# Optimization experiments

Measured on AMD Instinct MI355X. Metric: run time of the kernel, lower is better.

The kernel has to match this reference:

```python
import jax, jax.numpy as jnp
import numpy as np

B, LQ, LT, D = 16, 576, 512, 768
H, DH = 12, 64
TOPK = 64
GATE_INIT = -4.0
EPS = 1e-5


def _layernorm(x, g, b):
    m = jnp.mean(x, axis=-1, keepdims=True)
    v = jnp.mean(jnp.square(x - m), axis=-1, keepdims=True)
    return (x - m) * jax.lax.rsqrt(v + EPS) * g + b


def setup_inputs() -> dict:
    key = jax.random.key(0)
    ks = jax.random.split(key, 8)
    s = D ** -0.5
    return {
        "x_q": jax.random.normal(ks[0], (B, LQ, D), jnp.float32),
        "x_kv": jax.random.normal(ks[1], (B, LT, D), jnp.float32),
        "kv_attn_mask": jnp.ones((B, LT), jnp.int32),
        "wq": jax.random.normal(ks[2], (D, D), jnp.float32) * s,
        "wk": jax.random.normal(ks[3], (D, D), jnp.float32) * s,
        "wv": jax.random.normal(ks[4], (D, D), jnp.float32) * s,
        "wo": jax.random.normal(ks[5], (D, D), jnp.float32) * s,
        "ln_q_g": jnp.ones((D,), jnp.float32),
        "ln_q_b": jnp.zeros((D,), jnp.float32),
        "ln_kv_g": jnp.ones((D,), jnp.float32),
        "ln_kv_b": jnp.zeros((D,), jnp.float32),
        "head_queries": jax.random.normal(ks[6], (H, DH), jnp.float32) * DH ** -0.5,
        "resid_logit": jnp.asarray(GATE_INIT, jnp.float32),
    }


def reference(x_q, x_kv, kv_attn_mask, wq, wk, wv, wo,
              ln_q_g, ln_q_b, ln_kv_g, ln_kv_b, head_queries, resid_logit):
    scale = DH ** -0.5
    Bc, Lq, _ = x_q.shape
    Lt = x_kv.shape[1]
    xq_n = _layernorm(x_q, ln_q_g, ln_q_b)
    xkv_n = _layernorm(x_kv, ln_kv_g, ln_kv_b)
    # torch Linear: y = x @ W.T
    q = (xq_n @ wq.T).reshape(Bc, Lq, H, DH).transpose(0, 2, 1, 3)   # [B,H,Lq,DH]
    k = (xkv_n @ wk.T).reshape(Bc, Lt, H, DH).transpose(0, 2, 1, 3)  # [B,H,Lt,DH]
    v = (xkv_n @ wv.T).reshape(Bc, Lt, H, DH).transpose(0, 2, 1, 3)

    valid = (kv_attn_mask != 0)  # [B,Lt]
    neg = jnp.asarray(-jnp.inf, q.dtype)

    # head-wise gate from learned head queries attending over keys
    gate_scores = jnp.einsum('hd,bhld->bhl', head_queries, k) * scale  # [B,H,Lt]
    gate_scores = jnp.where(valid[:, None, :], gate_scores, neg)
    gate_attn = jax.nn.softmax(gate_scores, axis=-1)
    c_h = jnp.einsum('bhl,bhld->bhd', gate_attn, k)
    g_logits = jnp.einsum('bhd,hd->bh', c_h, head_queries) * scale
    g_h = jax.nn.sigmoid(g_logits)[:, :, None, None]  # [B,H,1,1]

    # top-k token routing: zero out non-selected K/V (matches torch.where -> zeros)
    if TOPK and TOPK < Lt:
        _, topk_idx = jax.lax.top_k(gate_scores, TOPK)  # [B,H,K]
        keep = jax.nn.one_hot(topk_idx, Lt, dtype=q.dtype).sum(axis=-2) > 0  # [B,H,Lt]
        k = jnp.where(keep[..., None], k, 0.0)
        v = jnp.where(keep[..., None], v, 0.0)

    attn_logits = jnp.einsum('bhqd,bhkd->bhqk', q, k) * scale  # [B,H,Lq,Lt]
    attn_logits = jnp.where(valid[:, None, None, :], attn_logits, neg)
    attn = jax.nn.softmax(attn_logits, axis=-1)
    out = jnp.einsum('bhqk,bhkd->bhqd', attn, v) * g_h
    out = out.transpose(0, 2, 1, 3).reshape(Bc, Lq, H * DH)
    out = out @ wo.T
    alpha = jax.nn.sigmoid(resid_logit)
    return x_q + alpha * out
```

## Files before the change

kernel.cpp:

```cpp
#include <hip/hip_runtime.h>
#include <math.h>

#define BB 16
#define LQ 576
#define LT 512
#define DD 768
#define HH 12
#define DH 64
#define TOPK 64

typedef __attribute__((ext_vector_type(8))) short bf16x8;
typedef __attribute__((ext_vector_type(4))) float f32x4;
typedef __attribute__((ext_vector_type(4))) unsigned short u16x4;

static constexpr size_t XQBF  = 0;
static constexpr size_t XKVBF = 3538944;
static constexpr size_t WQB   = 6684672;
static constexpr size_t WKB   = 6979584;
static constexpr size_t WVB   = 7274496;
static constexpr size_t WOB   = 7569408;
static constexpr size_t QBFo  = 7864320;
static constexpr size_t UBo   = 11403264;
static constexpr size_t GSo   = 11409408;
static constexpr size_t IDXo  = 17694720;
static constexpr size_t VBIA  = 17707008;
static constexpr size_t NDVo  = 17719296;
static constexpr size_t GHo   = 17719488;
static constexpr size_t KCo   = 17719680;
static constexpr size_t VCTo  = 18112896;

__device__ inline unsigned short f2bf(float f) {
  union { float f; unsigned u; } v; v.f = f;
  unsigned r = v.u + 0x7FFFu + ((v.u >> 16) & 1u);
  return (unsigned short)(r >> 16);
}
__device__ inline float bf2f(unsigned short u) {
  union { unsigned u; float f; } v; v.u = ((unsigned)u) << 16;
  return v.f;
}
__device__ inline void gload_lds16(const void* src, void* dst) {
  __builtin_amdgcn_global_load_lds((const __attribute__((address_space(1))) void*)src,
                                   (__attribute__((address_space(3))) void*)dst, 16, 0, 0);
}

__global__ __launch_bounds__(256) void ln_all(const float* __restrict__ xq,
                                              const float* __restrict__ xkv,
                                              const float* __restrict__ gq,
                                              const float* __restrict__ bq,
                                              const float* __restrict__ gkv,
                                              const float* __restrict__ bkv,
                                              unsigned short* __restrict__ yq,
                                              unsigned short* __restrict__ ykv) {
  int row = blockIdx.x;
  const float *xr, *gg, *bb;
  unsigned short* yr;
  if (row < BB * LQ) {
    xr = xq + (size_t)row * DD; gg = gq; bb = bq; yr = yq + (size_t)row * DD;
  } else {
    int r = row - BB * LQ;
    xr = xkv + (size_t)r * DD; gg = gkv; bb = bkv; yr = ykv + (size_t)r * DD;
  }
  int t = threadIdx.x;
  float v0 = xr[t], v1 = xr[t + 256], v2 = xr[t + 512];
  __shared__ float red[4];
  float s = v0 + v1 + v2;
  #pragma unroll
  for (int o = 32; o > 0; o >>= 1) s += __shfl_xor(s, o);
  if ((t & 63) == 0) red[t >> 6] = s;
  __syncthreads();
  float m = (red[0] + red[1] + red[2] + red[3]) * (1.0f / 768.0f);
  float d0 = v0 - m, d1 = v1 - m, d2 = v2 - m;
  float s2 = d0 * d0 + d1 * d1 + d2 * d2;
  #pragma unroll
  for (int o = 32; o > 0; o >>= 1) s2 += __shfl_xor(s2, o);
  __syncthreads();
  if ((t & 63) == 0) red[t >> 6] = s2;
  __syncthreads();
  float var = (red[0] + red[1] + red[2] + red[3]) * (1.0f / 768.0f);
  float rs = rsqrtf(var + 1e-5f);
  yr[t]       = f2bf(d0 * rs * gg[t]       + bb[t]);
  yr[t + 256] = f2bf(d1 * rs * gg[t + 256] + bb[t + 256]);
  yr[t + 512] = f2bf(d2 * rs * gg[t + 512] + bb[t + 512]);
}

__global__ __launch_bounds__(256) void conv4u(const float* __restrict__ s0, const float* __restrict__ s1,
                                              const float* __restrict__ s2, const float* __restrict__ s3,
                                              unsigned short* d0, unsigned short* d1,
                                              unsigned short* d2, unsigned short* d3,
                                              const float* __restrict__ hq,
                                              unsigned short* __restrict__ UB) {
  int t = threadIdx.x;
  if (blockIdx.y == 4) {
    int h = blockIdx.x;
    if (h >= 16) return;
    if (h < HH) {
      float a0 = 0.0f, a1 = 0.0f, a2 = 0.0f;
      for (int d = 0; d < DH; ++d) {
        float sc = hq[h * DH + d];
        const float* wr = s1 + (size_t)(h * DH + d) * DD;
        a0 += sc * wr[t]; a1 += sc * wr[t + 256]; a2 += sc * wr[t + 512];
      }
      UB[h * DD + t]       = f2bf(a0 * 0.125f);
      UB[h * DD + t + 256] = f2bf(a1 * 0.125f);
      UB[h * DD + t + 512] = f2bf(a2 * 0.125f);
    } else {
      UB[h * DD + t] = 0; UB[h * DD + t + 256] = 0; UB[h * DD + t + 512] = 0;
    }
    return;
  }
  const float* s; unsigned short* d;
  switch (blockIdx.y) {
    case 0: s = s0; d = d0; break;
    case 1: s = s1; d = d1; break;
    case 2: s = s2; d = d2; break;
    default: s = s3; d = d3; break;
  }
  int i = (blockIdx.x * 256 + t) * 4;
  float4 v = *reinterpret_cast<const float4*>(&s[i]);
  u16x4 o = { f2bf(v.x), f2bf(v.y), f2bf(v.z), f2bf(v.w) };
  *reinterpret_cast<u16x4*>(&d[i]) = o;
}

#define COMMON_PREAMBLE()                                                      \
  const int tid = threadIdx.x;                                                 \
  const int w = tid >> 6, l = tid & 63;                                        \
  const int lq = l & 15, g = l >> 4;                                           \
  const int srow = l >> 3;                                                     \
  const int scol = ((l & 7) * 16) ^ ((srow & 7) << 4);


#define QO_STAGE(BUFI, T)                                                      \
  {                                                                            \
    int k0s = (T) * 64;                                                        \
    _Pragma("unroll")                                                          \
    for (int it = 0; it < 2; ++it)                                             \
      gload_lds16(Asrc + (size_t)it * 8 * DD + k0s, &As[BUFI][(w * 16 + it * 8) * 64]); \
    _Pragma("unroll")                                                          \
    for (int jt = 0; jt < 4; ++jt)                                             \
      gload_lds16(Bsrc + (size_t)jt * 8 * DD + k0s, &Bs[BUFI][(w * 32 + jt * 8) * 64]); \
  }

#define QO_COMPUTE(BUFI)                                                       \
  {                                                                            \
    bf16x8 a[2][2], b[4][2];                                                   \
    _Pragma("unroll")                                                          \
    for (int mi = 0; mi < 2; ++mi)                                             \
      _Pragma("unroll")                                                        \
      for (int ks = 0; ks < 2; ++ks)                                           \
        a[mi][ks] = *reinterpret_cast<const bf16x8*>(&As[BUFI][aoff[mi][ks]]); \
    _Pragma("unroll")                                                          \
    for (int ni = 0; ni < 4; ++ni)                                             \
      _Pragma("unroll")                                                        \
      for (int ks = 0; ks < 2; ++ks)                                           \
        b[ni][ks] = *reinterpret_cast<const bf16x8*>(&Bs[BUFI][boff[ni][ks]]); \
    _Pragma("unroll")                                                          \
    for (int ks = 0; ks < 2; ++ks)                                             \
      _Pragma("unroll")                                                        \
      for (int mi = 0; mi < 2; ++mi)                                           \
        _Pragma("unroll")                                                      \
        for (int ni = 0; ni < 4; ++ni)                                         \
          acc[mi][ni] = __builtin_amdgcn_mfma_f32_16x16x32_bf16(               \
              a[mi][ks], b[ni][ks], acc[mi][ni], 0, 0, 0);                     \
  }

#define QO_MAIN()                                                              \
  const int wr = w >> 1, wc = w & 1;                                           \
  int aoff[2][2], boff[4][2];                                                  \
  _Pragma("unroll")                                                            \
  for (int mi = 0; mi < 2; ++mi) {                                             \
    int rowa = wr * 32 + mi * 16 + lq;                                         \
    _Pragma("unroll")                                                          \
    for (int ks = 0; ks < 2; ++ks)                                             \
      aoff[mi][ks] = rowa * 64 + (((ks * 64 + g * 16) ^ ((rowa & 7) << 4)) >> 1); \
  }                                                                            \
  _Pragma("unroll")                                                            \
  for (int ni = 0; ni < 4; ++ni) {                                             \
    int rowb = wc * 64 + ni * 16 + lq;                                         \
    _Pragma("unroll")                                                          \
    for (int ks = 0; ks < 2; ++ks)                                             \
      boff[ni][ks] = rowb * 64 + (((ks * 64 + g * 16) ^ ((rowb & 7) << 4)) >> 1); \
  }                                                                            \
  QO_STAGE(0, 0);                                                              \
  QO_STAGE(1, 1);                                                              \
  _Pragma("unroll")                                                            \
  for (int t = 0; t < 12; ++t) {                                               \
    if (t < 11) asm volatile("s_waitcnt vmcnt(6)" ::: "memory");               \
    else        asm volatile("s_waitcnt vmcnt(0)" ::: "memory");               \
    __builtin_amdgcn_sched_barrier(0);                                         \
    __builtin_amdgcn_s_barrier();                                              \
    if ((t & 1) == 0) { QO_COMPUTE(0); } else { QO_COMPUTE(1); }               \
    __builtin_amdgcn_s_barrier();                                              \
    __builtin_amdgcn_sched_barrier(0);                                         \
    if (t + 2 < 12) {                                                          \
      if ((t & 1) == 0) { QO_STAGE(0, t + 2); } else { QO_STAGE(1, t + 2); }   \
    }                                                                          \
  }

__global__ __launch_bounds__(256, 3) void q_gemm(const unsigned short* __restrict__ xqb,
                                                 const unsigned short* __restrict__ wqb,
                                                 unsigned short* __restrict__ QBF) {
  __shared__ __align__(16) unsigned short As[2][64 * 64];
  __shared__ __align__(16) unsigned short Bs[2][128 * 64];
  COMMON_PREAMBLE();
  int p = blockIdx.x;
  int bid = (p & 7) * 108 + (p >> 3);
  const int mtile = bid / 6, nt = bid % 6;
  const int bm = mtile * 64, bn = nt * 128;
  const unsigned short* Asrc = xqb + (size_t)(bm + w * 16 + srow) * DD + (scol >> 1);
  const unsigned short* Bsrc = wqb + (size_t)(bn + w * 32 + srow) * DD + (scol >> 1);
  f32x4 acc[2][4] = {};
  QO_MAIN();
  const int m_base = bm + wr * 32, n_base = bn + wc * 64;
  #pragma unroll
  for (int mi = 0; mi < 2; ++mi)
    #pragma unroll
    for (int r = 0; r < 4; ++r) {
      int m = m_base + mi * 16 + g * 4 + r;
      #pragma unroll
      for (int ni = 0; ni < 4; ++ni) {
        int n = n_base + ni * 16 + lq;
        QBF[(size_t)m * DD + n] = f2bf(acc[mi][ni][r] * 0.125f);
      }
    }
}

__global__ __launch_bounds__(256, 3) void o_gemm(const unsigned short* __restrict__ ABF,
                                                 const unsigned short* __restrict__ wob,
                                                 float* __restrict__ out,
                                                 const float* __restrict__ resid,
                                                 const float* __restrict__ gl) {
  __shared__ __align__(16) unsigned short As[2][64 * 64];
  __shared__ __align__(16) unsigned short Bs[2][128 * 64];
  COMMON_PREAMBLE();
  int p = blockIdx.x;
  int bid = (p & 7) * 108 + (p >> 3);
  const int mtile = bid / 6, nt = bid % 6;
  const int bm = mtile * 64, bn = nt * 128;
  const unsigned short* Asrc = ABF + (size_t)(bm + w * 16 + srow) * DD + (scol >> 1);
  const unsigned short* Bsrc = wob + (size_t)(bn + w * 32 + srow) * DD + (scol >> 1);
  f32x4 acc[2][4] = {};
  QO_MAIN();
  float alpha = 1.0f / (1.0f + __expf(-gl[0]));
  const int m_base = bm + wr * 32, n_base = bn + wc * 64;
  #pragma unroll
  for (int mi = 0; mi < 2; ++mi)
    #pragma unroll
    for (int r = 0; r < 4; ++r) {
      int m = m_base + mi * 16 + g * 4 + r;
      #pragma unroll
      for (int ni = 0; ni < 4; ++ni) {
        int n = n_base + ni * 16 + lq;
        out[(size_t)m * DD + n] = resid[(size_t)m * DD + n] + alpha * acc[mi][ni][r];
      }
    }
}

__global__ __launch_bounds__(256) void gs_gemm(const unsigned short* __restrict__ xkvb,
                                               const unsigned short* __restrict__ UB,
                                               float* __restrict__ GS) {
  __shared__ __align__(16) unsigned short Xs[2][64 * 64];
  __shared__ __align__(16) unsigned short Us[2][16 * 64];
  COMMON_PREAMBLE();
  const int bm = blockIdx.x * 64;
  const unsigned short* Asrc = xkvb + (size_t)(bm + srow) * DD + (scol >> 1);
  const unsigned short* Us0 = UB + (size_t)srow * DD + (scol >> 1);
  const unsigned short* Us1 = UB + (size_t)(8 + srow) * DD + (scol >> 1);

#define GS_STAGE(BUFI, T)                                                      \
  {                                                                            \
    int k0s = (T) * 64;                                                        \
    _Pragma("unroll")                                                          \
    for (int it = 0; it < 2; ++it) {                                           \
      int rbase = it * 32 + w * 8;                                             \
      gload_lds16(Asrc + (size_t)rbase * DD + k0s, &Xs[BUFI][rbase * 64]);     \
    }                                                                          \
    gload_lds16(Us0 + k0s, &Us[BUFI][0]);                                      \
    gload_lds16(Us1 + k0s, &Us[BUFI][8 * 64]);                                 \
  }

  f32x4 acc = {};

#define GS_COMPUTE(BUFI)                                                       \
  {                                                                            \
    _Pragma("unroll")                                                          \
    for (int ks = 0; ks < 2; ++ks) {                                           \
      int arow = w * 16 + lq;                                                  \
      int acb = (ks * 64 + g * 16) ^ ((arow & 7) << 4);                        \
      bf16x8 a = *reinterpret_cast<const bf16x8*>(&Xs[BUFI][arow * 64 + (acb >> 1)]); \
      int brow = lq;                                                           \
      int bcb = (ks * 64 + g * 16) ^ ((brow & 7) << 4);                        \
      bf16x8 b = *reinterpret_cast<const bf16x8*>(&Us[BUFI][brow * 64 + (bcb >> 1)]); \
      acc = __builtin_amdgcn_mfma_f32_16x16x32_bf16(a, b, acc, 0, 0, 0);       \
    }                                                                          \
  }

  GS_STAGE(0, 0);
  GS_STAGE(1, 1);
  #pragma unroll
  for (int t = 0; t < 12; ++t) {
    if (t < 11) asm volatile("s_waitcnt vmcnt(4)" ::: "memory");
    else        asm volatile("s_waitcnt vmcnt(0)" ::: "memory");
    __builtin_amdgcn_sched_barrier(0);
    __builtin_amdgcn_s_barrier();
    if ((t & 1) == 0) { GS_COMPUTE(0); } else { GS_COMPUTE(1); }
    __builtin_amdgcn_s_barrier();
    __builtin_amdgcn_sched_barrier(0);
    if (t + 2 < 12) {
      if ((t & 1) == 0) { GS_STAGE(0, t + 2); } else { GS_STAGE(1, t + 2); }
    }
  }
  #pragma unroll
  for (int r = 0; r < 4; ++r)
    GS[(size_t)(bm + w * 16 + g * 4 + r) * 16 + lq] = acc[r];
}

__global__ __launch_bounds__(512) void gate_topk(const float* __restrict__ GS,
                                                 const int* __restrict__ mask,
                                                 int* __restrict__ idxo,
                                                 float* __restrict__ vbias,
                                                 float* __restrict__ ndv,
                                                 float* __restrict__ g_h) {
  int bh = blockIdx.x, b = bh / HH, h = bh % HH;
  int l = threadIdx.x;
  __shared__ float s_sc[512];
  __shared__ float red[8];
  __shared__ int wred[8];
  float sc = GS[(size_t)(b * LT + l) * 16 + h];
  bool maskv = (mask[b * LT + l] != 0);
  if (!maskv) sc = -INFINITY;
  s_sc[l] = sc;
  float m0 = sc;
  #pragma unroll
  for (int o = 32; o > 0; o >>= 1) m0 = fmaxf(m0, __shfl_xor(m0, o));
  if ((l & 63) == 0) red[l >> 6] = m0;
  __syncthreads();
  float m = red[0];
  #pragma unroll
  for (int w = 1; w < 8; w++) m = fmaxf(m, red[w]);
  float p = __expf(sc - m);
  float s1 = p;
  #pragma unroll
  for (int o = 32; o > 0; o >>= 1) s1 += __shfl_xor(s1, o);
  __syncthreads();
  if ((l & 63) == 0) red[l >> 6] = s1;
  __syncthreads();
  float Z = 0.0f;
  #pragma unroll
  for (int w = 0; w < 8; w++) Z += red[w];
  p /= Z;
  float gc = maskv ? p * sc : 0.0f;
  #pragma unroll
  for (int o = 32; o > 0; o >>= 1) gc += __shfl_xor(gc, o);
  __syncthreads();
  if ((l & 63) == 0) red[l >> 6] = gc;
  __syncthreads();
  if (l == 0) {
    float G = 0.0f;
    #pragma unroll
    for (int w = 0; w < 8; w++) G += red[w];
    g_h[bh] = 1.0f / (1.0f + __expf(-G));
  }
  float my = s_sc[l];
  int cnt = 0;
  for (int j = 0; j < LT; j++) {
    float sj = s_sc[j];
    cnt += (sj > my || (sj == my && j < l)) ? 1 : 0;
  }
  if (cnt < TOPK) {
    idxo[bh * TOPK + cnt] = l;
    vbias[bh * TOPK + cnt] = maskv ? 0.0f : -INFINITY;
  }
  int dv = (maskv && cnt >= TOPK) ? 1 : 0;
  unsigned long long bal = __ballot(dv);
  if ((l & 63) == 0) wred[l >> 6] = __popcll(bal);
  __syncthreads();
  if (l == 0) {
    int nd = 0;
    #pragma unroll
    for (int w = 0; w < 8; w++) nd += wred[w];
    ndv[bh] = (float)nd;
  }
}

__global__ __launch_bounds__(256, 2) void kvc_gemm(const unsigned short* __restrict__ xkvb,
                                                   const unsigned short* __restrict__ wkb,
                                                   const unsigned short* __restrict__ wvb,
                                                   const int* __restrict__ idxo,
                                                   unsigned short* __restrict__ KC,
                                                   unsigned short* __restrict__ VCT) {
  __shared__ __align__(16) unsigned short Xs[2][4096];
  __shared__ __align__(16) unsigned short Ks[2][4096];
  __shared__ __align__(16) unsigned short Vs[2][4096];
  __shared__ int sidx[64];
  COMMON_PREAMBLE();
  const int bh = blockIdx.x, b = bh / HH, h = bh % HH;
  if (tid < 64) sidx[tid] = idxo[bh * TOPK + tid];
  __syncthreads();
  const int j0 = w * 16 + srow, j1 = w * 16 + 8 + srow;
  const unsigned short* xs0 = xkvb + (size_t)(b * LT + sidx[j0]) * DD + (scol >> 1);
  const unsigned short* xs1 = xkvb + (size_t)(b * LT + sidx[j1]) * DD + (scol >> 1);
  const unsigned short* wk0 = wkb + (size_t)(h * DH + j0) * DD + (scol >> 1);
  const unsigned short* wk1 = wkb + (size_t)(h * DH + j1) * DD + (scol >> 1);
  const unsigned short* wv0 = wvb + (size_t)(h * DH + j0) * DD + (scol >> 1);
  const unsigned short* wv1 = wvb + (size_t)(h * DH + j1) * DD + (scol >> 1);

#define KV_STAGE(BUFI, T)                                                      \
    {                                                                          \
      int k0s = (T) * 64;                                                      \
      gload_lds16(xs0 + k0s, &Xs[BUFI][(w * 16) * 64]);                        \
      gload_lds16(xs1 + k0s, &Xs[BUFI][(w * 16 + 8) * 64]);                    \
      gload_lds16(wk0 + k0s, &Ks[BUFI][(w * 16) * 64]);                        \
      gload_lds16(wk1 + k0s, &Ks[BUFI][(w * 16 + 8) * 64]);                    \
      gload_lds16(wv0 + k0s, &Vs[BUFI][(w * 16) * 64]);                        \
      gload_lds16(wv1 + k0s, &Vs[BUFI][(w * 16 + 8) * 64]);                    \
    }

  f32x4 accK[4] = {}, accV[4] = {};

#define KV_COMPUTE(BUFI)                                                       \
    {                                                                          \
      _Pragma("unroll")                                                        \
      for (int ks = 0; ks < 2; ++ks) {                                         \
        int arow = w * 16 + lq;                                                \
        int acb = (ks * 64 + g * 16) ^ ((arow & 7) << 4);                      \
        bf16x8 ax = *reinterpret_cast<const bf16x8*>(&Xs[BUFI][arow * 64 + (acb >> 1)]); \
        bf16x8 av = *reinterpret_cast<const bf16x8*>(&Vs[BUFI][arow * 64 + (acb >> 1)]); \
        _Pragma("unroll")                                                      \
        for (int ni = 0; ni < 4; ++ni) {                                       \
          int brow = ni * 16 + lq;                                             \
          int bcb = (ks * 64 + g * 16) ^ ((brow & 7) << 4);                    \
          bf16x8 bk = *reinterpret_cast<const bf16x8*>(&Ks[BUFI][brow * 64 + (bcb >> 1)]); \
          accK[ni] = __builtin_amdgcn_mfma_f32_16x16x32_bf16(ax, bk, accK[ni], 0, 0, 0); \
          bf16x8 bx = *reinterpret_cast<const bf16x8*>(&Xs[BUFI][brow * 64 + (bcb >> 1)]); \
          accV[ni] = __builtin_amdgcn_mfma_f32_16x16x32_bf16(av, bx, accV[ni], 0, 0, 0); \
        }                                                                      \
      }                                                                        \
    }

  KV_STAGE(0, 0);
  KV_STAGE(1, 1);
  #pragma unroll
  for (int t = 0; t < 12; ++t) {
    if (t < 11) asm volatile("s_waitcnt vmcnt(6)" ::: "memory");
    else        asm volatile("s_waitcnt vmcnt(0)" ::: "memory");
    __builtin_amdgcn_sched_barrier(0);
    __builtin_amdgcn_s_barrier();
    if ((t & 1) == 0) { KV_COMPUTE(0); } else { KV_COMPUTE(1); }
    __builtin_amdgcn_s_barrier();
    __builtin_amdgcn_sched_barrier(0);
    if (t + 2 < 12) {
      if ((t & 1) == 0) { KV_STAGE(0, t + 2); } else { KV_STAGE(1, t + 2); }
    }
  }
  #pragma unroll
  for (int ni = 0; ni < 4; ++ni)
    #pragma unroll
    for (int r = 0; r < 4; ++r) {
      int mrow = w * 16 + g * 4 + r;
      KC [(size_t)bh * 4096 + mrow * 64 + ni * 16 + lq] = f2bf(accK[ni][r]);
      VCT[(size_t)bh * 4096 + mrow * 64 + ni * 16 + lq] = f2bf(accV[ni][r]);
    }
}

__global__ __launch_bounds__(256) void attn_topk(const unsigned short* __restrict__ Qb,
                                                 const unsigned short* __restrict__ KC,
                                                 const unsigned short* __restrict__ VCT,
                                                 const float* __restrict__ vbias,
                                                 const float* __restrict__ ndv,
                                                 const float* __restrict__ g_h,
                                                 unsigned short* __restrict__ att) {
  const int bh = blockIdx.y, b = bh / HH, h = bh % HH;
  const int q0 = blockIdx.x * 64;
  const int tid = threadIdx.x;
  const int w = tid >> 6, l = tid & 63;
  const int lq = l & 15, g = l >> 4;

  __shared__ __align__(16) unsigned short Klds[64 * 64];
  __shared__ __align__(16) unsigned short Vlds[64 * 64];
  __shared__ float svb[64];

  const int srow = l >> 3;
  const int scol = ((l & 7) * 16) ^ ((srow & 7) << 4);
  #pragma unroll
  for (int it = 0; it < 2; ++it) {
    int rbase = w * 16 + it * 8;
    gload_lds16(KC  + (size_t)bh * 4096 + (rbase + srow) * 64 + (scol >> 1), &Klds[rbase * 64]);
    gload_lds16(VCT + (size_t)bh * 4096 + (rbase + srow) * 64 + (scol >> 1), &Vlds[rbase * 64]);
  }
  if (tid < 64) svb[tid] = vbias[bh * TOPK + tid];

  bf16x8 qf0, qf1;
  {
    const unsigned short* qrow =
        Qb + ((size_t)(b * LQ + q0 + w * 16 + lq)) * DD + h * DH + g * 8;
    qf0 = *reinterpret_cast<const bf16x8*>(qrow);
    qf1 = *reinterpret_cast<const bf16x8*>(qrow + 32);
  }
  __syncthreads();

  f32x4 S[4];
  #pragma unroll
  for (int kt = 0; kt < 4; ++kt) {
    f32x4 acc = {};
    int row = kt * 16 + lq;
    int c0 = (g * 16) ^ ((row & 7) << 4);
    int c1 = (64 + g * 16) ^ ((row & 7) << 4);
    bf16x8 a0 = *reinterpret_cast<const bf16x8*>(&Klds[row * 64 + (c0 >> 1)]);
    bf16x8 a1 = *reinterpret_cast<const bf16x8*>(&Klds[row * 64 + (c1 >> 1)]);
    acc = __builtin_amdgcn_mfma_f32_16x16x32_bf16(a0, qf0, acc, 0, 0, 0);
    acc = __builtin_amdgcn_mfma_f32_16x16x32_bf16(a1, qf1, acc, 0, 0, 0);
    S[kt] = acc;
  }

  float s_v[16];
  float mx = -INFINITY;
  #pragma unroll
  for (int kt = 0; kt < 4; ++kt)
    #pragma unroll
    for (int r = 0; r < 4; ++r) {
      float s = S[kt][r] + svb[kt * 16 + g * 4 + r];
      s_v[kt * 4 + r] = s;
      mx = fmaxf(mx, s);
    }
  mx = fmaxf(mx, __shfl_xor(mx, 16));
  mx = fmaxf(mx, __shfl_xor(mx, 32));
  float nd = ndv[bh];
  float m2 = (nd > 0.0f) ? fmaxf(mx, 0.0f) : mx;

  float psum = 0.0f;
  unsigned short pb[16];
  #pragma unroll
  for (int i = 0; i < 16; ++i) {
    float p = __expf(s_v[i] - m2);
    psum += p;
    pb[i] = f2bf(p);
  }
  psum += __shfl_xor(psum, 16);
  psum += __shfl_xor(psum, 32);
  float Z = psum + nd * __expf(-m2);
  float inv = 1.0f / Z;

  bf16x8 pa0, pa1;
  #pragma unroll
  for (int j = 0; j < 8; ++j) { pa0[j] = (short)pb[j]; pa1[j] = (short)pb[8 + j]; }

  f32x4 O[4] = {};
  #pragma unroll
  for (int dt = 0; dt < 4; ++dt) {
    int r = dt * 16 + lq;
    int swz = (r & 7) << 4;
    #pragma unroll
    for (int ks = 0; ks < 2; ++ks) {
      int cl = (64 * ks + g * 8) ^ swz;
      int ch = (64 * ks + 32 + g * 8) ^ swz;
      u16x4 lo = *reinterpret_cast<const u16x4*>(&Vlds[r * 64 + (cl >> 1)]);
      u16x4 hi = *reinterpret_cast<const u16x4*>(&Vlds[r * 64 + (ch >> 1)]);
      bf16x8 vb = { (short)lo[0], (short)lo[1], (short)lo[2], (short)lo[3],
                    (short)hi[0], (short)hi[1], (short)hi[2], (short)hi[3] };
      O[dt] = __builtin_amdgcn_mfma_f32_16x16x32_bf16(ks == 0 ? pa0 : pa1, vb, O[dt], 0, 0, 0);
    }
  }

  float invl[4];
  #pragma unroll
  for (int r = 0; r < 4; ++r) invl[r] = __shfl(inv, g * 4 + r);
  float gh = g_h[bh];
  #pragma unroll
  for (int dt = 0; dt < 4; ++dt)
    #pragma unroll
    for (int r = 0; r < 4; ++r) {
      int q = q0 + w * 16 + g * 4 + r;
      att[((size_t)(b * LQ + q)) * DD + h * DH + dt * 16 + lq] =
          f2bf(O[dt][r] * invl[r] * gh);
    }
}

extern "C" void kernel_launch(void* const* d_in, const int* in_sizes, int n_in,
                              void* d_out, int out_size, void* d_ws, size_t ws_size,
                              hipStream_t stream) {
  const float* x_q      = (const float*)d_in[0];
  const float* x_kv     = (const float*)d_in[1];
  const int*   mask     = (const int*)d_in[2];
  const float* wq       = (const float*)d_in[3];
  const float* wk       = (const float*)d_in[4];
  const float* wv       = (const float*)d_in[5];
  const float* wo       = (const float*)d_in[6];
  const float* ln_q_g   = (const float*)d_in[7];
  const float* ln_q_b   = (const float*)d_in[8];
  const float* ln_kv_g  = (const float*)d_in[9];
  const float* ln_kv_b  = (const float*)d_in[10];
  const float* hq       = (const float*)d_in[11];
  const float* resid_l  = (const float*)d_in[12];
  float* out = (float*)d_out;
  float* ws  = (float*)d_ws;

  unsigned short* xqb  = (unsigned short*)(ws + XQBF);
  unsigned short* xkvb = (unsigned short*)(ws + XKVBF);
  unsigned short* wqb  = (unsigned short*)(ws + WQB);
  unsigned short* wkb  = (unsigned short*)(ws + WKB);
  unsigned short* wvb  = (unsigned short*)(ws + WVB);
  unsigned short* wob  = (unsigned short*)(ws + WOB);
  unsigned short* QBF  = (unsigned short*)(ws + QBFo);
  unsigned short* UB   = (unsigned short*)(ws + UBo);
  float*          GS   = (float*)(ws + GSo);
  int*            IDX  = (int*)(ws + IDXo);
  unsigned short* KC   = (unsigned short*)(ws + KCo);
  unsigned short* VCT  = (unsigned short*)(ws + VCTo);
  unsigned short* ABF  = xqb;

  conv4u<<<dim3(576, 5), dim3(256), 0, stream>>>(wq, wk, wv, wo, wqb, wkb, wvb, wob, hq, UB);

  ln_all<<<dim3(BB * LQ + BB * LT), dim3(256), 0, stream>>>(x_q, x_kv, ln_q_g, ln_q_b,
                                                            ln_kv_g, ln_kv_b, xqb, xkvb);

  gs_gemm<<<dim3(128), dim3(256), 0, stream>>>(xkvb, UB, GS);

  gate_topk<<<dim3(BB * HH), dim3(512), 0, stream>>>(GS, mask, IDX,
                                                     ws + VBIA, ws + NDVo, ws + GHo);

  q_gemm<<<dim3(864), dim3(256), 0, stream>>>(xqb, wqb, QBF);

  kvc_gemm<<<dim3(BB * HH), dim3(256), 0, stream>>>(xkvb, wkb, wvb, IDX, KC, VCT);

  attn_topk<<<dim3(LQ / 64, BB * HH), dim3(256), 0, stream>>>(QBF, KC, VCT,
                                                              ws + VBIA, ws + NDVo, ws + GHo, ABF);

  o_gemm<<<dim3(864), dim3(256), 0, stream>>>(ABF, wob, out, x_q, resid_l);
}
```

Measured before the change: 119.8 us.

## Merge Q projection and compacted KV GEMM into one launch with triple buffering

```diff
diff --git a/kernel.cpp b/kernel.cpp
--- a/kernel.cpp
+++ b/kernel.cpp
@@ -129,30 +129,30 @@
   const int scol = ((l & 7) * 16) ^ ((srow & 7) << 4);
 
 
-#define QO_STAGE(BUFI, T)                                                      \
+#define QO_STAGE(AB, BBP, T)                                                   \
   {                                                                            \
     int k0s = (T) * 64;                                                        \
     _Pragma("unroll")                                                          \
     for (int it = 0; it < 2; ++it)                                             \
-      gload_lds16(Asrc + (size_t)it * 8 * DD + k0s, &As[BUFI][(w * 16 + it * 8) * 64]); \
+      gload_lds16(Asrc + (size_t)it * 8 * DD + k0s, (AB) + (w * 16 + it * 8) * 64); \
     _Pragma("unroll")                                                          \
     for (int jt = 0; jt < 4; ++jt)                                             \
-      gload_lds16(Bsrc + (size_t)jt * 8 * DD + k0s, &Bs[BUFI][(w * 32 + jt * 8) * 64]); \
-  }
-
-#define QO_COMPUTE(BUFI)                                                       \
+      gload_lds16(Bsrc + (size_t)jt * 8 * DD + k0s, (BBP) + (w * 32 + jt * 8) * 64); \
+  }
+
+#define QO_COMPUTE(AB, BBP)                                                    \
   {                                                                            \
     bf16x8 a[2][2], b[4][2];                                                   \
     _Pragma("unroll")                                                          \
     for (int mi = 0; mi < 2; ++mi)                                             \
       _Pragma("unroll")                                                        \
       for (int ks = 0; ks < 2; ++ks)                                           \
-        a[mi][ks] = *reinterpret_cast<const bf16x8*>(&As[BUFI][aoff[mi][ks]]); \
+        a[mi][ks] = *reinterpret_cast<const bf16x8*>((AB) + aoff[mi][ks]);     \
     _Pragma("unroll")                                                          \
     for (int ni = 0; ni < 4; ++ni)                                             \
       _Pragma("unroll")                                                        \
       for (int ks = 0; ks < 2; ++ks)                                           \
-        b[ni][ks] = *reinterpret_cast<const bf16x8*>(&Bs[BUFI][boff[ni][ks]]); \
+        b[ni][ks] = *reinterpret_cast<const bf16x8*>((BBP) + boff[ni][ks]);    \
     _Pragma("unroll")                                                          \
     for (int ks = 0; ks < 2; ++ks)                                             \
       _Pragma("unroll")                                                        \
@@ -180,57 +180,141 @@
     for (int ks = 0; ks < 2; ++ks)                                             \
       boff[ni][ks] = rowb * 64 + (((ks * 64 + g * 16) ^ ((rowb & 7) << 4)) >> 1); \
   }                                                                            \
-  QO_STAGE(0, 0);                                                              \
-  QO_STAGE(1, 1);                                                              \
+  QO_STAGE(S + 0 * 4096, S + 12288 + 0 * 8192, 0);                             \
+  QO_STAGE(S + 1 * 4096, S + 12288 + 1 * 8192, 1);                             \
+  QO_STAGE(S + 2 * 4096, S + 12288 + 2 * 8192, 2);                             \
   _Pragma("unroll")                                                            \
   for (int t = 0; t < 12; ++t) {                                               \
-    if (t < 11) asm volatile("s_waitcnt vmcnt(6)" ::: "memory");               \
-    else        asm volatile("s_waitcnt vmcnt(0)" ::: "memory");               \
+    if (t <= 9)       asm volatile("s_waitcnt vmcnt(12)" ::: "memory");        \
+    else if (t == 10) asm volatile("s_waitcnt vmcnt(6)" ::: "memory");         \
+    else              asm volatile("s_waitcnt vmcnt(0)" ::: "memory");         \
     __builtin_amdgcn_sched_barrier(0);                                         \
     __builtin_amdgcn_s_barrier();                                              \
-    if ((t & 1) == 0) { QO_COMPUTE(0); } else { QO_COMPUTE(1); }               \
+    QO_COMPUTE(S + (t % 3) * 4096, S + 12288 + (t % 3) * 8192);                \
     __builtin_amdgcn_s_barrier();                                              \
     __builtin_amdgcn_sched_barrier(0);                                         \
-    if (t + 2 < 12) {                                                          \
-      if ((t & 1) == 0) { QO_STAGE(0, t + 2); } else { QO_STAGE(1, t + 2); }   \
+    if (t + 3 < 12) {                                                          \
+      QO_STAGE(S + (t % 3) * 4096, S + 12288 + (t % 3) * 8192, t + 3);         \
     }                                                                          \
   }
 
-__global__ __launch_bounds__(256, 3) void q_gemm(const unsigned short* __restrict__ xqb,
+__global__ __launch_bounds__(256, 2) void proj2f(const unsigned short* __restrict__ xqb,
                                                  const unsigned short* __restrict__ wqb,
-                                                 unsigned short* __restrict__ QBF) {
-  __shared__ __align__(16) unsigned short As[2][64 * 64];
-  __shared__ __align__(16) unsigned short Bs[2][128 * 64];
+                                                 const unsigned short* __restrict__ xkvb,
+                                                 const unsigned short* __restrict__ wkb,
+                                                 const unsigned short* __restrict__ wvb,
+                                                 const int* __restrict__ idxo,
+                                                 unsigned short* __restrict__ QBF,
+                                                 unsigned short* __restrict__ KC,
+                                                 unsigned short* __restrict__ VCT) {
+  __shared__ __align__(16) unsigned short S[36864];
+  __shared__ int sidx[64];
   COMMON_PREAMBLE();
   int p = blockIdx.x;
-  int bid = (p & 7) * 108 + (p >> 3);
-  const int mtile = bid / 6, nt = bid % 6;
-  const int bm = mtile * 64, bn = nt * 128;
-  const unsigned short* Asrc = xqb + (size_t)(bm + w * 16 + srow) * DD + (scol >> 1);
-  const unsigned short* Bsrc = wqb + (size_t)(bn + w * 32 + srow) * DD + (scol >> 1);
-  f32x4 acc[2][4] = {};
-  QO_MAIN();
-  const int m_base = bm + wr * 32, n_base = bn + wc * 64;
-  #pragma unroll
-  for (int mi = 0; mi < 2; ++mi)
-    #pragma unroll
-    for (int r = 0; r < 4; ++r) {
-      int m = m_base + mi * 16 + g * 4 + r;
+  int bid = (p & 7) * 132 + (p >> 3);
+
+  if (bid < 864) {
+    const int mtile = bid / 6, nt = bid % 6;
+    const int bm = mtile * 64, bn = nt * 128;
+    const unsigned short* Asrc = xqb + (size_t)(bm + w * 16 + srow) * DD + (scol >> 1);
+    const unsigned short* Bsrc = wqb + (size_t)(bn + w * 32 + srow) * DD + (scol >> 1);
+    f32x4 acc[2][4] = {};
+    QO_MAIN();
+    const int m_base = bm + wr * 32, n_base = bn + wc * 64;
+    #pragma unroll
+    for (int mi = 0; mi < 2; ++mi)
       #pragma unroll
-      for (int ni = 0; ni < 4; ++ni) {
-        int n = n_base + ni * 16 + lq;
-        QBF[(size_t)m * DD + n] = f2bf(acc[mi][ni][r] * 0.125f);
+      for (int r = 0; r < 4; ++r) {
+        int m = m_base + mi * 16 + g * 4 + r;
+        #pragma unroll
+        for (int ni = 0; ni < 4; ++ni) {
+          int n = n_base + ni * 16 + lq;
+          QBF[(size_t)m * DD + n] = f2bf(acc[mi][ni][r] * 0.125f);
+        }
       }
-    }
-}
-
-__global__ __launch_bounds__(256, 3) void o_gemm(const unsigned short* __restrict__ ABF,
+  } else {
+    const int bh = bid - 864, b = bh / HH, h = bh % HH;
+    if (tid < 64) sidx[tid] = idxo[bh * TOPK + tid];
+    __syncthreads();
+    const int j0 = w * 16 + srow, j1 = w * 16 + 8 + srow;
+    const unsigned short* xs0 = xkvb + (size_t)(b * LT + sidx[j0]) * DD + (scol >> 1);
+    const unsigned short* xs1 = xkvb + (size_t)(b * LT + sidx[j1]) * DD + (scol >> 1);
+    const unsigned short* wk0 = wkb + (size_t)(h * DH + j0) * DD + (scol >> 1);
+    const unsigned short* wk1 = wkb + (size_t)(h * DH + j1) * DD + (scol >> 1);
+    const unsigned short* wv0 = wvb + (size_t)(h * DH + j0) * DD + (scol >> 1);
+    const unsigned short* wv1 = wvb + (size_t)(h * DH + j1) * DD + (scol >> 1);
+
+#define KV_STAGE3(T)                                                           \
+    {                                                                          \
+      int k0s = (T) * 64;                                                      \
+      unsigned short* Xd = S + ((T) % 3) * 4096;                               \
+      unsigned short* Kd = S + 12288 + ((T) % 3) * 4096;                       \
+      unsigned short* Vd = S + 24576 + ((T) % 3) * 4096;                       \
+      gload_lds16(xs0 + k0s, Xd + (w * 16) * 64);                              \
+      gload_lds16(xs1 + k0s, Xd + (w * 16 + 8) * 64);                          \
+      gload_lds16(wk0 + k0s, Kd + (w * 16) * 64);                              \
+      gload_lds16(wk1 + k0s, Kd + (w * 16 + 8) * 64);                          \
+      gload_lds16(wv0 + k0s, Vd + (w * 16) * 64);                              \
+      gload_lds16(wv1 + k0s, Vd + (w * 16 + 8) * 64);                          \
+    }
+
+    f32x4 accK[4] = {}, accV[4] = {};
+
+#define KV_COMPUTE3(T)                                                         \
+    {                                                                          \
+      const unsigned short* Xd = S + ((T) % 3) * 4096;                         \
+      const unsigned short* Kd = S + 12288 + ((T) % 3) * 4096;                 \
+      const unsigned short* Vd = S + 24576 + ((T) % 3) * 4096;                 \
+      _Pragma("unroll")                                                        \
+      for (int ks = 0; ks < 2; ++ks) {                                         \
+        int arow = w * 16 + lq;                                                \
+        int acb = (ks * 64 + g * 16) ^ ((arow & 7) << 4);                      \
+        bf16x8 ax = *reinterpret_cast<const bf16x8*>(Xd + arow * 64 + (acb >> 1)); \
+        bf16x8 av = *reinterpret_cast<const bf16x8*>(Vd + arow * 64 + (acb >> 1)); \
+        _Pragma("unroll")                                                      \
+        for (int ni = 0; ni < 4; ++ni) {                                       \
+          int brow = ni * 16 + lq;                                             \
+          int bcb = (ks * 64 + g * 16) ^ ((brow & 7) << 4);                    \
+          bf16x8 bk = *reinterpret_cast<const bf16x8*>(Kd + brow * 64 + (bcb >> 1)); \
+          accK[ni] = __builtin_amdgcn_mfma_f32_16x16x32_bf16(ax, bk, accK[ni], 0, 0, 0); \
+          bf16x8 bx = *reinterpret_cast<const bf16x8*>(Xd + brow * 64 + (bcb >> 1)); \
+          accV[ni] = __builtin_amdgcn_mfma_f32_16x16x32_bf16(av, bx, accV[ni], 0, 0, 0); \
+        }                                                                      \
+      }                                                                        \
+    }
+
+    KV_STAGE3(0);
+    KV_STAGE3(1);
+    KV_STAGE3(2);
+    #pragma unroll
+    for (int t = 0; t < 12; ++t) {
+      if (t <= 9)       asm volatile("s_waitcnt vmcnt(12)" ::: "memory");
+      else if (t == 10) asm volatile("s_waitcnt vmcnt(6)" ::: "memory");
+      else              asm volatile("s_waitcnt vmcnt(0)" ::: "memory");
+      __builtin_amdgcn_sched_barrier(0);
+      __builtin_amdgcn_s_barrier();
+      KV_COMPUTE3(t);
+      __builtin_amdgcn_s_barrier();
+      __builtin_amdgcn_sched_barrier(0);
+      if (t + 3 < 12) KV_STAGE3(t + 3);
+    }
+    #pragma unroll
+    for (int ni = 0; ni < 4; ++ni)
+      #pragma unroll
+      for (int r = 0; r < 4; ++r) {
+        int mrow = w * 16 + g * 4 + r;
+        KC [(size_t)bh * 4096 + mrow * 64 + ni * 16 + lq] = f2bf(accK[ni][r]);
+        VCT[(size_t)bh * 4096 + mrow * 64 + ni * 16 + lq] = f2bf(accV[ni][r]);
+      }
+  }
+}
+
+__global__ __launch_bounds__(256, 2) void o_gemm(const unsigned short* __restrict__ ABF,
                                                  const unsigned short* __restrict__ wob,
                                                  float* __restrict__ out,
                                                  const float* __restrict__ resid,
                                                  const float* __restrict__ gl) {
-  __shared__ __align__(16) unsigned short As[2][64 * 64];
-  __shared__ __align__(16) unsigned short Bs[2][128 * 64];
+  __shared__ __align__(16) unsigned short S[36864];
   COMMON_PREAMBLE();
   int p = blockIdx.x;
   int bid = (p & 7) * 108 + (p >> 3);
@@ -380,86 +464,6 @@
     for (int w = 0; w < 8; w++) nd += wred[w];
     ndv[bh] = (float)nd;
   }
-}
-
-__global__ __launch_bounds__(256, 2) void kvc_gemm(const unsigned short* __restrict__ xkvb,
-                                                   const unsigned short* __restrict__ wkb,
-                                                   const unsigned short* __restrict__ wvb,
-                                                   const int* __restrict__ idxo,
-                                                   unsigned short* __restrict__ KC,
-                                                   unsigned short* __restrict__ VCT) {
-  __shared__ __align__(16) unsigned short Xs[2][4096];
-  __shared__ __align__(16) unsigned short Ks[2][4096];
-  __shared__ __align__(16) unsigned short Vs[2][4096];
-  __shared__ int sidx[64];
-  COMMON_PREAMBLE();
-  const int bh = blockIdx.x, b = bh / HH, h = bh % HH;
-  if (tid < 64) sidx[tid] = idxo[bh * TOPK + tid];
-  __syncthreads();
-  const int j0 = w * 16 + srow, j1 = w * 16 + 8 + srow;
-  const unsigned short* xs0 = xkvb + (size_t)(b * LT + sidx[j0]) * DD + (scol >> 1);
-  const unsigned short* xs1 = xkvb + (size_t)(b * LT + sidx[j1]) * DD + (scol >> 1);
-  const unsigned short* wk0 = wkb + (size_t)(h * DH + j0) * DD + (scol >> 1);
-  const unsigned short* wk1 = wkb + (size_t)(h * DH + j1) * DD + (scol >> 1);
-  const unsigned short* wv0 = wvb + (size_t)(h * DH + j0) * DD + (scol >> 1);
-  const unsigned short* wv1 = wvb + (size_t)(h * DH + j1) * DD + (scol >> 1);
-
-#define KV_STAGE(BUFI, T)                                                      \
-    {                                                                          \
-      int k0s = (T) * 64;                                                      \
-      gload_lds16(xs0 + k0s, &Xs[BUFI][(w * 16) * 64]);                        \
-      gload_lds16(xs1 + k0s, &Xs[BUFI][(w * 16 + 8) * 64]);                    \
-      gload_lds16(wk0 + k0s, &Ks[BUFI][(w * 16) * 64]);                        \
-      gload_lds16(wk1 + k0s, &Ks[BUFI][(w * 16 + 8) * 64]);                    \
-      gload_lds16(wv0 + k0s, &Vs[BUFI][(w * 16) * 64]);                        \
-      gload_lds16(wv1 + k0s, &Vs[BUFI][(w * 16 + 8) * 64]);                    \
-    }
-
-  f32x4 accK[4] = {}, accV[4] = {};
-
-#define KV_COMPUTE(BUFI)                                                       \
-    {                                                                          \
-      _Pragma("unroll")                                                        \
-      for (int ks = 0; ks < 2; ++ks) {                                         \
-        int arow = w * 16 + lq;                                                \
-        int acb = (ks * 64 + g * 16) ^ ((arow & 7) << 4);                      \
-        bf16x8 ax = *reinterpret_cast<const bf16x8*>(&Xs[BUFI][arow * 64 + (acb >> 1)]); \
-        bf16x8 av = *reinterpret_cast<const bf16x8*>(&Vs[BUFI][arow * 64 + (acb >> 1)]); \
-        _Pragma("unroll")                                                      \
-        for (int ni = 0; ni < 4; ++ni) {                                       \
-          int brow = ni * 16 + lq;                                             \
-          int bcb = (ks * 64 + g * 16) ^ ((brow & 7) << 4);                    \
-          bf16x8 bk = *reinterpret_cast<const bf16x8*>(&Ks[BUFI][brow * 64 + (bcb >> 1)]); \
-          accK[ni] = __builtin_amdgcn_mfma_f32_16x16x32_bf16(ax, bk, accK[ni], 0, 0, 0); \
-          bf16x8 bx = *reinterpret_cast<const bf16x8*>(&Xs[BUFI][brow * 64 + (bcb >> 1)]); \
-          accV[ni] = __builtin_amdgcn_mfma_f32_16x16x32_bf16(av, bx, accV[ni], 0, 0, 0); \
-        }                                                                      \
-      }                                                                        \
-    }
-
-  KV_STAGE(0, 0);
-  KV_STAGE(1, 1);
-  #pragma unroll
-  for (int t = 0; t < 12; ++t) {
-    if (t < 11) asm volatile("s_waitcnt vmcnt(6)" ::: "memory");
-    else        asm volatile("s_waitcnt vmcnt(0)" ::: "memory");
-    __builtin_amdgcn_sched_barrier(0);
-    __builtin_amdgcn_s_barrier();
-    if ((t & 1) == 0) { KV_COMPUTE(0); } else { KV_COMPUTE(1); }
-    __builtin_amdgcn_s_barrier();
-    __builtin_amdgcn_sched_barrier(0);
-    if (t + 2 < 12) {
-      if ((t & 1) == 0) { KV_STAGE(0, t + 2); } else { KV_STAGE(1, t + 2); }
-    }
-  }
-  #pragma unroll
-  for (int ni = 0; ni < 4; ++ni)
-    #pragma unroll
-    for (int r = 0; r < 4; ++r) {
-      int mrow = w * 16 + g * 4 + r;
-      KC [(size_t)bh * 4096 + mrow * 64 + ni * 16 + lq] = f2bf(accK[ni][r]);
-      VCT[(size_t)bh * 4096 + mrow * 64 + ni * 16 + lq] = f2bf(accV[ni][r]);
-    }
 }
 
 __global__ __launch_bounds__(256) void attn_topk(const unsigned short* __restrict__ Qb,
@@ -618,9 +622,7 @@
   gate_topk<<<dim3(BB * HH), dim3(512), 0, stream>>>(GS, mask, IDX,
                                                      ws + VBIA, ws + NDVo, ws + GHo);
 
-  q_gemm<<<dim3(864), dim3(256), 0, stream>>>(xqb, wqb, QBF);
-
-  kvc_gemm<<<dim3(BB * HH), dim3(256), 0, stream>>>(xkvb, wkb, wvb, IDX, KC, VCT);
+  proj2f<<<dim3(1056), dim3(256), 0, stream>>>(xqb, wqb, xkvb, wkb, wvb, IDX, QBF, KC, VCT);
 
   attn_topk<<<dim3(LQ / 64, BB * HH), dim3(256), 0, stream>>>(QBF, KC, VCT,
                                                               ws + VBIA, ws + NDVo, ws + GHo, ABF);
```

New measurement: 117.2 us. 2.2% less time.

## Restructure Q/O GEMMs to stage full weight panel in LDS, stream A from registers

Applied to the files above, without the earlier changes.

```diff
diff --git a/kernel.cpp b/kernel.cpp
--- a/kernel.cpp
+++ b/kernel.cpp
@@ -129,128 +129,95 @@
   const int scol = ((l & 7) * 16) ^ ((srow & 7) << 4);
 
 
-#define QO_STAGE(BUFI, T)                                                      \
+#define PANEL_STAGE(WSRC, BN)                                                  \
   {                                                                            \
-    int k0s = (T) * 64;                                                        \
+    int rowl = l >> 3;                                                         \
+    int colb = ((l & 7) * 16) ^ ((rowl & 7) << 4);                             \
     _Pragma("unroll")                                                          \
-    for (int it = 0; it < 2; ++it)                                             \
-      gload_lds16(Asrc + (size_t)it * 8 * DD + k0s, &As[BUFI][(w * 16 + it * 8) * 64]); \
+    for (int i = 0; i < 12; ++i) {                                             \
+      int idx = w * 12 + i;                                                    \
+      int j = idx >> 3, rg = idx & 7;                                          \
+      gload_lds16(WSRC + (size_t)((BN) + rg * 8 + rowl) * DD + j * 64 + (colb >> 1), \
+                  &Bp[idx * 512]);                                             \
+    }                                                                          \
+  }
+
+#define PANEL_LOOP(APTR)                                                       \
+  const unsigned short* a0p = (APTR) + (size_t)(bm + w * 32 + lq) * DD + g * 8; \
+  const unsigned short* a1p = a0p + (size_t)16 * DD;                           \
+  f32x4 acc[2][4] = {};                                                        \
+  bf16x8 a0 = *reinterpret_cast<const bf16x8*>(a0p);                           \
+  bf16x8 a1 = *reinterpret_cast<const bf16x8*>(a1p);                           \
+  _Pragma("unroll")                                                            \
+  for (int s = 0; s < 24; ++s) {                                               \
+    bf16x8 a0n = a0, a1n = a1;                                                 \
+    if (s + 1 < 24) {                                                          \
+      a0n = *reinterpret_cast<const bf16x8*>(a0p + (s + 1) * 32);              \
+      a1n = *reinterpret_cast<const bf16x8*>(a1p + (s + 1) * 32);              \
+    }                                                                          \
     _Pragma("unroll")                                                          \
-    for (int jt = 0; jt < 4; ++jt)                                             \
-      gload_lds16(Bsrc + (size_t)jt * 8 * DD + k0s, &Bs[BUFI][(w * 32 + jt * 8) * 64]); \
-  }
-
-#define QO_COMPUTE(BUFI)                                                       \
-  {                                                                            \
-    bf16x8 a[2][2], b[4][2];                                                   \
-    _Pragma("unroll")                                                          \
-    for (int mi = 0; mi < 2; ++mi)                                             \
-      _Pragma("unroll")                                                        \
-      for (int ks = 0; ks < 2; ++ks)                                           \
-        a[mi][ks] = *reinterpret_cast<const bf16x8*>(&As[BUFI][aoff[mi][ks]]); \
-    _Pragma("unroll")                                                          \
-    for (int ni = 0; ni < 4; ++ni)                                             \
-      _Pragma("unroll")                                                        \
-      for (int ks = 0; ks < 2; ++ks)                                           \
-        b[ni][ks] = *reinterpret_cast<const bf16x8*>(&Bs[BUFI][boff[ni][ks]]); \
-    _Pragma("unroll")                                                          \
-    for (int ks = 0; ks < 2; ++ks)                                             \
-      _Pragma("unroll")                                                        \
-      for (int mi = 0; mi < 2; ++mi)                                           \
-        _Pragma("unroll")                                                      \
-        for (int ni = 0; ni < 4; ++ni)                                         \
-          acc[mi][ni] = __builtin_amdgcn_mfma_f32_16x16x32_bf16(               \
-              a[mi][ks], b[ni][ks], acc[mi][ni], 0, 0, 0);                     \
-  }
-
-#define QO_MAIN()                                                              \
-  const int wr = w >> 1, wc = w & 1;                                           \
-  int aoff[2][2], boff[4][2];                                                  \
-  _Pragma("unroll")                                                            \
-  for (int mi = 0; mi < 2; ++mi) {                                             \
-    int rowa = wr * 32 + mi * 16 + lq;                                         \
-    _Pragma("unroll")                                                          \
-    for (int ks = 0; ks < 2; ++ks)                                             \
-      aoff[mi][ks] = rowa * 64 + (((ks * 64 + g * 16) ^ ((rowa & 7) << 4)) >> 1); \
-  }                                                                            \
-  _Pragma("unroll")                                                            \
-  for (int ni = 0; ni < 4; ++ni) {                                             \
-    int rowb = wc * 64 + ni * 16 + lq;                                         \
-    _Pragma("unroll")                                                          \
-    for (int ks = 0; ks < 2; ++ks)                                             \
-      boff[ni][ks] = rowb * 64 + (((ks * 64 + g * 16) ^ ((rowb & 7) << 4)) >> 1); \
-  }                                                                            \
-  QO_STAGE(0, 0);                                                              \
-  QO_STAGE(1, 1);                                                              \
-  _Pragma("unroll")                                                            \
-  for (int t = 0; t < 12; ++t) {                                               \
-    if (t < 11) asm volatile("s_waitcnt vmcnt(6)" ::: "memory");               \
-    else        asm volatile("s_waitcnt vmcnt(0)" ::: "memory");               \
-    __builtin_amdgcn_sched_barrier(0);                                         \
-    __builtin_amdgcn_s_barrier();                                              \
-    if ((t & 1) == 0) { QO_COMPUTE(0); } else { QO_COMPUTE(1); }               \
-    __builtin_amdgcn_s_barrier();                                              \
-    __builtin_amdgcn_sched_barrier(0);                                         \
-    if (t + 2 < 12) {                                                          \
-      if ((t & 1) == 0) { QO_STAGE(0, t + 2); } else { QO_STAGE(1, t + 2); }   \
+    for (int ni = 0; ni < 4; ++ni) {                                           \
+      int r = ni * 16 + lq;                                                    \
+      int offb = (((s & 1) * 64 + g * 16) ^ ((r & 7) << 4));                   \
+      bf16x8 b = *reinterpret_cast<const bf16x8*>(                             \
+          &Bp[(s >> 1) * 4096 + r * 64 + (offb >> 1)]);                        \
+      acc[0][ni] = __builtin_amdgcn_mfma_f32_16x16x32_bf16(a0, b, acc[0][ni], 0, 0, 0); \
+      acc[1][ni] = __builtin_amdgcn_mfma_f32_16x16x32_bf16(a1, b, acc[1][ni], 0, 0, 0); \
     }                                                                          \
-  }
-
-__global__ __launch_bounds__(256, 3) void q_gemm(const unsigned short* __restrict__ xqb,
-                                                 const unsigned short* __restrict__ wqb,
-                                                 unsigned short* __restrict__ QBF) {
-  __shared__ __align__(16) unsigned short As[2][64 * 64];
-  __shared__ __align__(16) unsigned short Bs[2][128 * 64];
-  COMMON_PREAMBLE();
+    a0 = a0n; a1 = a1n;                                                        \
+  }
+
+__global__ __launch_bounds__(512) void q_gemm(const unsigned short* __restrict__ A,
+                                              const unsigned short* __restrict__ W,
+                                              unsigned short* __restrict__ QBF) {
+  __shared__ __align__(16) unsigned short Bp[12 * 4096];
+  const int tid = threadIdx.x;
+  const int w = tid >> 6, l = tid & 63;
+  const int lq = l & 15, g = l >> 4;
   int p = blockIdx.x;
-  int bid = (p & 7) * 108 + (p >> 3);
-  const int mtile = bid / 6, nt = bid % 6;
-  const int bm = mtile * 64, bn = nt * 128;
-  const unsigned short* Asrc = xqb + (size_t)(bm + w * 16 + srow) * DD + (scol >> 1);
-  const unsigned short* Bsrc = wqb + (size_t)(bn + w * 32 + srow) * DD + (scol >> 1);
-  f32x4 acc[2][4] = {};
-  QO_MAIN();
-  const int m_base = bm + wr * 32, n_base = bn + wc * 64;
+  int bid = (p & 7) * 54 + (p >> 3);
+  const int mtile = bid / 12, nt = bid % 12;
+  const int bm = mtile * 256, bn = nt * 64;
+  PANEL_STAGE(W, bn);
+  __syncthreads();
+  PANEL_LOOP(A);
   #pragma unroll
   for (int mi = 0; mi < 2; ++mi)
     #pragma unroll
-    for (int r = 0; r < 4; ++r) {
-      int m = m_base + mi * 16 + g * 4 + r;
+    for (int rr = 0; rr < 4; ++rr) {
+      int m = bm + w * 32 + mi * 16 + g * 4 + rr;
+      #pragma unroll
+      for (int ni = 0; ni < 4; ++ni)
+        QBF[(size_t)m * DD + bn + ni * 16 + lq] = f2bf(acc[mi][ni][rr] * 0.125f);
+    }
+}
+
+__global__ __launch_bounds__(512) void o_gemm(const unsigned short* __restrict__ A,
+                                              const unsigned short* __restrict__ W,
+                                              float* __restrict__ out,
+                                              const float* __restrict__ resid,
+                                              const float* __restrict__ gl) {
+  __shared__ __align__(16) unsigned short Bp[12 * 4096];
+  const int tid = threadIdx.x;
+  const int w = tid >> 6, l = tid & 63;
+  const int lq = l & 15, g = l >> 4;
+  int p = blockIdx.x;
+  int bid = (p & 7) * 54 + (p >> 3);
+  const int mtile = bid / 12, nt = bid % 12;
+  const int bm = mtile * 256, bn = nt * 64;
+  PANEL_STAGE(W, bn);
+  __syncthreads();
+  PANEL_LOOP(A);
+  float alpha = 1.0f / (1.0f + __expf(-gl[0]));
+  #pragma unroll
+  for (int mi = 0; mi < 2; ++mi)
+    #pragma unroll
+    for (int rr = 0; rr < 4; ++rr) {
+      int m = bm + w * 32 + mi * 16 + g * 4 + rr;
       #pragma unroll
       for (int ni = 0; ni < 4; ++ni) {
-        int n = n_base + ni * 16 + lq;
-        QBF[(size_t)m * DD + n] = f2bf(acc[mi][ni][r] * 0.125f);
-      }
-    }
-}
-
-__global__ __launch_bounds__(256, 3) void o_gemm(const unsigned short* __restrict__ ABF,
-                                                 const unsigned short* __restrict__ wob,
-                                                 float* __restrict__ out,
-                                                 const float* __restrict__ resid,
-                                                 const float* __restrict__ gl) {
-  __shared__ __align__(16) unsigned short As[2][64 * 64];
-  __shared__ __align__(16) unsigned short Bs[2][128 * 64];
-  COMMON_PREAMBLE();
-  int p = blockIdx.x;
-  int bid = (p & 7) * 108 + (p >> 3);
-  const int mtile = bid / 6, nt = bid % 6;
-  const int bm = mtile * 64, bn = nt * 128;
-  const unsigned short* Asrc = ABF + (size_t)(bm + w * 16 + srow) * DD + (scol >> 1);
-  const unsigned short* Bsrc = wob + (size_t)(bn + w * 32 + srow) * DD + (scol >> 1);
-  f32x4 acc[2][4] = {};
-  QO_MAIN();
-  float alpha = 1.0f / (1.0f + __expf(-gl[0]));
-  const int m_base = bm + wr * 32, n_base = bn + wc * 64;
-  #pragma unroll
-  for (int mi = 0; mi < 2; ++mi)
-    #pragma unroll
-    for (int r = 0; r < 4; ++r) {
-      int m = m_base + mi * 16 + g * 4 + r;
-      #pragma unroll
-      for (int ni = 0; ni < 4; ++ni) {
-        int n = n_base + ni * 16 + lq;
-        out[(size_t)m * DD + n] = resid[(size_t)m * DD + n] + alpha * acc[mi][ni][r];
+        int n = bn + ni * 16 + lq;
+        out[(size_t)m * DD + n] = resid[(size_t)m * DD + n] + alpha * acc[mi][ni][rr];
       }
     }
 }
@@ -618,12 +585,12 @@
   gate_topk<<<dim3(BB * HH), dim3(512), 0, stream>>>(GS, mask, IDX,
                                                      ws + VBIA, ws + NDVo, ws + GHo);
 
-  q_gemm<<<dim3(864), dim3(256), 0, stream>>>(xqb, wqb, QBF);
+  q_gemm<<<dim3(432), dim3(512), 0, stream>>>(xqb, wqb, QBF);
 
   kvc_gemm<<<dim3(BB * HH), dim3(256), 0, stream>>>(xkvb, wkb, wvb, IDX, KC, VCT);
 
   attn_topk<<<dim3(LQ / 64, BB * HH), dim3(256), 0, stream>>>(QBF, KC, VCT,
                                                               ws + VBIA, ws + NDVo, ws + GHo, ABF);
 
-  o_gemm<<<dim3(864), dim3(256), 0, stream>>>(ABF, wob, out, x_q, resid_l);
-}
+  o_gemm<<<dim3(432), dim3(512), 0, stream>>>(ABF, wob, out, x_q, resid_l);
+}
```

Result: slower. 135.4 us (+13.0%).
